# Performance work log

Hardware: AMD Instinct MI355X
Metric: run time of the kernel (lower is better)

Reference implementation:

```python
import jax, jax.numpy as jnp
import numpy as np

TWO_N, D = 8192, 256
N = TWO_N // 2


def setup_inputs() -> dict:
    key = jax.random.key(0)
    k1, k2 = jax.random.split(key)
    embeddings = jax.random.normal(k1, (TWO_N, D), dtype=jnp.float32)
    pos_mask = jnp.zeros((N, TWO_N), dtype=bool)  # unused by the loss
    neg_mask = jax.random.randint(k2, (N, TWO_N), 0, 2).astype(bool)
    return {"embeddings": embeddings, "pos_mask": pos_mask, "neg_mask": neg_mask}


def reference(embeddings, pos_mask, neg_mask):
    # d[i, j] = <e_i, e_j>  (other_embeddings defaults to embeddings)
    d = jnp.matmul(embeddings, embeddings.T)            # [2N, 2N]
    n = embeddings.shape[0] // 2
    rows = d[:n]                                        # [N, 2N] (only rows 0..N-1 used)
    ap = rows[jnp.arange(n), jnp.arange(n) + n]         # d[i, i+N], shape [N]
    # masked sum_j exp(d[i,j] - ap_i) over negatives, then log(1 + .)
    expm = jnp.exp(rows - ap[:, None])                  # [N, 2N]
    j_all = jnp.log1p(jnp.sum(jnp.where(neg_mask, expm, 0.0), axis=1))  # [N]
    return jnp.mean(j_all)
```

## Files before the change

### kernel.cpp

```cpp
#include <hip/hip_runtime.h>
#include <math.h>

#define TWO_N 8192
#define NR 4096
#define D 256
#define BM 128
#define BN 128
#define BK 64

typedef __attribute__((ext_vector_type(8))) short bf16x8;
typedef __attribute__((ext_vector_type(4))) float f32x4;

#define AS1V const __attribute__((address_space(1))) void
#define AS3V __attribute__((address_space(3))) void

__device__ inline unsigned short f2bf(float x) {
  unsigned u = __builtin_bit_cast(unsigned, x);
  u += 0x7fffu + ((u >> 16) & 1u);
  return (unsigned short)(u >> 16);
}

__global__ void cvt_kernel(const float* __restrict__ emb, unsigned short* __restrict__ ebf) {
  const size_t i = ((size_t)blockIdx.x * 256 + threadIdx.x) * 8;
  const float4 a = *reinterpret_cast<const float4*>(emb + i);
  const float4 b = *reinterpret_cast<const float4*>(emb + i + 4);
  union { unsigned short s[8]; bf16x8 v; } o;
  o.s[0] = f2bf(a.x); o.s[1] = f2bf(a.y); o.s[2] = f2bf(a.z); o.s[3] = f2bf(a.w);
  o.s[4] = f2bf(b.x); o.s[5] = f2bf(b.y); o.s[6] = f2bf(b.z); o.s[7] = f2bf(b.w);
  *reinterpret_cast<bf16x8*>(ebf + i) = o.v;
}

__global__ void ap_zero_kernel(const float* __restrict__ emb, float* __restrict__ ap,
                               double* __restrict__ rowsum) {
  const int lane = threadIdx.x & 63;
  const int wid = threadIdx.x >> 6;
  const int i = blockIdx.x * 4 + wid;
  const float4 a = *reinterpret_cast<const float4*>(emb + (size_t)i * D + lane * 4);
  const float4 b = *reinterpret_cast<const float4*>(emb + (size_t)(i + NR) * D + lane * 4);
  float s = a.x * b.x + a.y * b.y + a.z * b.z + a.w * b.w;
#pragma unroll
  for (int off = 32; off >= 1; off >>= 1) s += __shfl_xor(s, off, 64);
  if (lane == 0) { ap[i] = s; rowsum[i] = 0.0; }
}

__global__ __launch_bounds__(256, 3) void fused_mfma(
    const unsigned short* __restrict__ ebf, const unsigned char* __restrict__ negm,
    const float* __restrict__ ap, double* __restrict__ rowsum) {
  __shared__ unsigned short As[BM * BK];
  __shared__ unsigned short Bs[BN * BK];
  const int t = threadIdx.x;
  const int lane = t & 63;
  const int wid = t >> 6;
  const int wr = wid >> 1;
  const int wc = wid & 1;
  const int sw = (blockIdx.x & 7) * 256 + (blockIdx.x >> 3);
  const int bi = sw >> 6;
  const int bj = sw & 63;

  f32x4 acc[4][4] = {};

  const int srow = lane >> 3;
  const int scol = (lane & 7) * 8;

  for (int kt = 0; kt < D / BK; ++kt) {
    const int k0 = kt * BK;
#pragma unroll
    for (int q = 0; q < 4; ++q) {
      const int rbase = wid * 32 + q * 8;
      const unsigned short* gA = ebf + (size_t)(bi * BM + rbase + srow) * D + k0 + scol;
      const unsigned short* gB = ebf + (size_t)(bj * BN + rbase + srow) * D + k0 + scol;
      __builtin_amdgcn_global_load_lds((AS1V*)gA, (AS3V*)(As + rbase * BK), 16, 0, 0);
      __builtin_amdgcn_global_load_lds((AS1V*)gB, (AS3V*)(Bs + rbase * BK), 16, 0, 0);
    }
    __syncthreads();
#pragma unroll
    for (int kk = 0; kk < 2; ++kk) {
      bf16x8 af[4], bfr[4];
      const int kof = kk * 32 + (lane >> 4) * 8;
#pragma unroll
      for (int m = 0; m < 4; ++m)
        af[m] = *reinterpret_cast<const bf16x8*>(&As[(wr * 64 + m * 16 + (lane & 15)) * BK + kof]);
#pragma unroll
      for (int n = 0; n < 4; ++n)
        bfr[n] = *reinterpret_cast<const bf16x8*>(&Bs[(wc * 64 + n * 16 + (lane & 15)) * BK + kof]);
#pragma unroll
      for (int m = 0; m < 4; ++m)
#pragma unroll
        for (int n = 0; n < 4; ++n)
          acc[m][n] = __builtin_amdgcn_mfma_f32_16x16x32_bf16(af[m], bfr[n], acc[m][n], 0, 0, 0);
    }
    __syncthreads();
  }

  const int g = lane >> 4;
  const int cl = lane & 15;
  double rs[4][4] = {};

#pragma unroll
  for (int m = 0; m < 4; ++m) {
    const int rowbase = bi * BM + wr * 64 + m * 16 + g * 4;
    float apv[4];
#pragma unroll
    for (int r2 = 0; r2 < 4; ++r2) apv[r2] = ap[rowbase + r2];
#pragma unroll
    for (int n = 0; n < 4; ++n) {
      const int col = bj * BN + wc * 64 + n * 16 + cl;
#pragma unroll
      for (int r2 = 0; r2 < 4; ++r2) {
        const unsigned char msk = negm[(size_t)(rowbase + r2) * TWO_N + col];
        const float x = acc[m][n][r2] - apv[r2];
        const float tt = x * 1.44269504088896340736f;
        const float kf = floorf(tt);
        const float mant = exp2f(tt - kf);
        const long long ebits = (long long)(1023 + (int)kf) << 52;
        const double sc = __builtin_bit_cast(double, ebits);
        rs[m][r2] += msk ? (double)mant * sc : 0.0;
      }
    }
  }
#pragma unroll
  for (int m = 0; m < 4; ++m)
#pragma unroll
    for (int r2 = 0; r2 < 4; ++r2) {
      double v = rs[m][r2];
#pragma unroll
      for (int off = 8; off >= 1; off >>= 1) v += __shfl_xor(v, off, 64);
      if (cl == 0) atomicAdd(&rowsum[bi * BM + wr * 64 + m * 16 + g * 4 + r2], v);
    }
}

__global__ void finalize_kernel(const double* __restrict__ rowsum, float* __restrict__ out) {
  __shared__ double red[4];
  const int t = threadIdx.x;
  double s = 0.0;
  for (int i = t; i < NR; i += 256) s += log1p(rowsum[i]);
#pragma unroll
  for (int off = 32; off >= 1; off >>= 1) s += __shfl_xor(s, off, 64);
  if ((t & 63) == 0) red[t >> 6] = s;
  __syncthreads();
  if (t == 0) out[0] = (float)((red[0] + red[1] + red[2] + red[3]) * (1.0 / NR));
}

extern "C" void kernel_launch(void* const* d_in, const int* in_sizes, int n_in,
                              void* d_out, int out_size, void* d_ws, size_t ws_size,
                              hipStream_t stream) {
  const float* emb = (const float*)d_in[0];
  const unsigned char* negm = (const unsigned char*)d_in[2];
  float* out = (float*)d_out;
  unsigned short* ebf = (unsigned short*)d_ws;
  float* ap = (float*)((char*)d_ws + (size_t)TWO_N * D * 2);
  double* rowsum = (double*)((char*)d_ws + (size_t)TWO_N * D * 2 + 16384);

  cvt_kernel<<<dim3(TWO_N * D / 8 / 256), dim3(256), 0, stream>>>(emb, ebf);
  ap_zero_kernel<<<dim3(NR / 4), dim3(256), 0, stream>>>(emb, ap, rowsum);
  fused_mfma<<<dim3((NR / BM) * (TWO_N / BN)), dim3(256), 0, stream>>>(ebf, negm, ap, rowsum);
  finalize_kernel<<<dim3(1), dim3(256), 0, stream>>>(rowsum, out);
}
```

Before: 296.9 us.

## Pack negative mask into bitwords and double-buffer LDS tiles in fused GEMM

Adds a repack kernel that compresses the byte-per-element negative mask into 64-bit bitmasks. The fused GEMM epilogue then reads one word per row per warp column instead of scattered byte loads. The GEMM main loop is also double-buffered in LDS so the next K tile loads while the current one computes, and occupancy hint drops to 2 blocks. The repack still reads the full mask once in a separate pass, so total mask traffic is not reduced, only access granularity.

```diff
diff --git a/kernel.cpp b/kernel.cpp
--- a/kernel.cpp
+++ b/kernel.cpp
@@ -7,6 +7,7 @@
 #define BM 128
 #define BN 128
 #define BK 64
+#define PMW (TWO_N / 64)
 
 typedef __attribute__((ext_vector_type(8))) short bf16x8;
 typedef __attribute__((ext_vector_type(4))) float f32x4;
@@ -30,6 +31,24 @@
   *reinterpret_cast<bf16x8*>(ebf + i) = o.v;
 }
 
+__global__ void repack_kernel(const unsigned char* __restrict__ negm,
+                              unsigned long long* __restrict__ pm) {
+  const int t = blockIdx.x * 256 + threadIdx.x;
+  const uint4* p = reinterpret_cast<const uint4*>(negm + (size_t)t * 64);
+  unsigned long long w = 0;
+#pragma unroll
+  for (int q = 0; q < 4; ++q) {
+    const uint4 v = p[q];
+    unsigned b = 0;
+    b |= (v.x & 1u) | ((v.x >> 7) & 2u) | ((v.x >> 14) & 4u) | ((v.x >> 21) & 8u);
+    b |= ((v.y & 1u) | ((v.y >> 7) & 2u) | ((v.y >> 14) & 4u) | ((v.y >> 21) & 8u)) << 4;
+    b |= ((v.z & 1u) | ((v.z >> 7) & 2u) | ((v.z >> 14) & 4u) | ((v.z >> 21) & 8u)) << 8;
+    b |= ((v.w & 1u) | ((v.w >> 7) & 2u) | ((v.w >> 14) & 4u) | ((v.w >> 21) & 8u)) << 12;
+    w |= (unsigned long long)b << (q * 16);
+  }
+  pm[t] = w;
+}
+
 __global__ void ap_zero_kernel(const float* __restrict__ emb, float* __restrict__ ap,
                                double* __restrict__ rowsum) {
   const int lane = threadIdx.x & 63;
@@ -43,11 +62,11 @@
   if (lane == 0) { ap[i] = s; rowsum[i] = 0.0; }
 }
 
-__global__ __launch_bounds__(256, 3) void fused_mfma(
-    const unsigned short* __restrict__ ebf, const unsigned char* __restrict__ negm,
+__global__ __launch_bounds__(256, 2) void fused_mfma(
+    const unsigned short* __restrict__ ebf, const unsigned long long* __restrict__ pm,
     const float* __restrict__ ap, double* __restrict__ rowsum) {
-  __shared__ unsigned short As[BM * BK];
-  __shared__ unsigned short Bs[BN * BK];
+  __shared__ unsigned short As[2][BM * BK];
+  __shared__ unsigned short Bs[2][BN * BK];
   const int t = threadIdx.x;
   const int lane = t & 63;
   const int wid = t >> 6;
@@ -62,27 +81,33 @@
   const int srow = lane >> 3;
   const int scol = (lane & 7) * 8;
 
-  for (int kt = 0; kt < D / BK; ++kt) {
+  auto STAGE = [&](int buf, int kt) {
     const int k0 = kt * BK;
 #pragma unroll
     for (int q = 0; q < 4; ++q) {
       const int rbase = wid * 32 + q * 8;
       const unsigned short* gA = ebf + (size_t)(bi * BM + rbase + srow) * D + k0 + scol;
       const unsigned short* gB = ebf + (size_t)(bj * BN + rbase + srow) * D + k0 + scol;
-      __builtin_amdgcn_global_load_lds((AS1V*)gA, (AS3V*)(As + rbase * BK), 16, 0, 0);
-      __builtin_amdgcn_global_load_lds((AS1V*)gB, (AS3V*)(Bs + rbase * BK), 16, 0, 0);
+      __builtin_amdgcn_global_load_lds((AS1V*)gA, (AS3V*)(As[buf] + rbase * BK), 16, 0, 0);
+      __builtin_amdgcn_global_load_lds((AS1V*)gB, (AS3V*)(Bs[buf] + rbase * BK), 16, 0, 0);
     }
-    __syncthreads();
+  };
+
+  STAGE(0, 0);
+  __syncthreads();
+  int cur = 0;
+  for (int kt = 0; kt < D / BK; ++kt) {
+    if (kt < D / BK - 1) STAGE(cur ^ 1, kt + 1);
 #pragma unroll
     for (int kk = 0; kk < 2; ++kk) {
       bf16x8 af[4], bfr[4];
       const int kof = kk * 32 + (lane >> 4) * 8;
 #pragma unroll
       for (int m = 0; m < 4; ++m)
-        af[m] = *reinterpret_cast<const bf16x8*>(&As[(wr * 64 + m * 16 + (lane & 15)) * BK + kof]);
+        af[m] = *reinterpret_cast<const bf16x8*>(&As[cur][(wr * 64 + m * 16 + (lane & 15)) * BK + kof]);
 #pragma unroll
       for (int n = 0; n < 4; ++n)
-        bfr[n] = *reinterpret_cast<const bf16x8*>(&Bs[(wc * 64 + n * 16 + (lane & 15)) * BK + kof]);
+        bfr[n] = *reinterpret_cast<const bf16x8*>(&Bs[cur][(wc * 64 + n * 16 + (lane & 15)) * BK + kof]);
 #pragma unroll
       for (int m = 0; m < 4; ++m)
 #pragma unroll
@@ -90,6 +115,7 @@
           acc[m][n] = __builtin_amdgcn_mfma_f32_16x16x32_bf16(af[m], bfr[n], acc[m][n], 0, 0, 0);
     }
     __syncthreads();
+    cur ^= 1;
   }
 
   const int g = lane >> 4;
@@ -99,21 +125,20 @@
 #pragma unroll
   for (int m = 0; m < 4; ++m) {
     const int rowbase = bi * BM + wr * 64 + m * 16 + g * 4;
-    float apv[4];
 #pragma unroll
-    for (int r2 = 0; r2 < 4; ++r2) apv[r2] = ap[rowbase + r2];
+    for (int r2 = 0; r2 < 4; ++r2) {
+      const int row = rowbase + r2;
+      const float apv = ap[row];
+      const unsigned long long mw = pm[(size_t)row * PMW + bj * 2 + wc];
 #pragma unroll
-    for (int n = 0; n < 4; ++n) {
-      const int col = bj * BN + wc * 64 + n * 16 + cl;
-#pragma unroll
-      for (int r2 = 0; r2 < 4; ++r2) {
-        const unsigned char msk = negm[(size_t)(rowbase + r2) * TWO_N + col];
-        const float x = acc[m][n][r2] - apv[r2];
+      for (int n = 0; n < 4; ++n) {
+        const float x = acc[m][n][r2] - apv;
         const float tt = x * 1.44269504088896340736f;
         const float kf = floorf(tt);
         const float mant = exp2f(tt - kf);
         const long long ebits = (long long)(1023 + (int)kf) << 52;
         const double sc = __builtin_bit_cast(double, ebits);
+        const bool msk = (mw >> (n * 16 + cl)) & 1;
         rs[m][r2] += msk ? (double)mant * sc : 0.0;
       }
     }
@@ -147,12 +172,15 @@
   const float* emb = (const float*)d_in[0];
   const unsigned char* negm = (const unsigned char*)d_in[2];
   float* out = (float*)d_out;
-  unsigned short* ebf = (unsigned short*)d_ws;
-  float* ap = (float*)((char*)d_ws + (size_t)TWO_N * D * 2);
-  double* rowsum = (double*)((char*)d_ws + (size_t)TWO_N * D * 2 + 16384);
+  char* ws = (char*)d_ws;
+  unsigned short* ebf = (unsigned short*)ws;
+  unsigned long long* pm = (unsigned long long*)(ws + (1u << 22));
+  float* ap = (float*)(ws + (2u << 22));
+  double* rowsum = (double*)(ws + (2u << 22) + 16384);
 
   cvt_kernel<<<dim3(TWO_N * D / 8 / 256), dim3(256), 0, stream>>>(emb, ebf);
+  repack_kernel<<<dim3(NR * PMW / 256), dim3(256), 0, stream>>>(negm, pm);
   ap_zero_kernel<<<dim3(NR / 4), dim3(256), 0, stream>>>(emb, ap, rowsum);
-  fused_mfma<<<dim3((NR / BM) * (TWO_N / BN)), dim3(256), 0, stream>>>(ebf, negm, ap, rowsum);
+  fused_mfma<<<dim3((NR / BM) * (TWO_N / BN)), dim3(256), 0, stream>>>(ebf, pm, ap, rowsum);
   finalize_kernel<<<dim3(1), dim3(256), 0, stream>>>(rowsum, out);
 }
```

Result: slower. 328.0 us (+10.5%).
